# Optimization experiments

Measured on AMD Instinct MI355X. Metric: run time of the kernel, lower is better.

## Reference

```python
import jax, jax.numpy as jnp
import numpy as np

DIM = 1024
CTX_DIM = 1024
HEADS = 16
HEAD_DIM = DIM // HEADS


def setup_inputs() -> dict:
    key = jax.random.key(0)
    ks = jax.random.split(key, 6)
    B, N, M = 4, 2048, 2048
    s = 0.02
    return {
        "x": jax.random.normal(ks[0], (B, N, DIM), dtype=jnp.float32),
        "context": jax.random.normal(ks[1], (B, M, CTX_DIM), dtype=jnp.float32),
        "Wq": jax.random.normal(ks[2], (DIM, DIM), dtype=jnp.float32) * s,
        "Wk": jax.random.normal(ks[3], (CTX_DIM, DIM), dtype=jnp.float32) * s,
        "Wv": jax.random.normal(ks[4], (CTX_DIM, DIM), dtype=jnp.float32) * s,
        "Wo": jax.random.normal(ks[5], (DIM, DIM), dtype=jnp.float32) * s,
        "bo": jnp.zeros((DIM,), dtype=jnp.float32),
    }


def reference(x, context, Wq, Wk, Wv, Wo, bo):
    B, N, C = x.shape
    scale = HEAD_DIM ** -0.5
    # projections then split heads: (B, H, N, Dh)
    q = (x @ Wq.T).reshape(B, N, HEADS, HEAD_DIM).transpose(0, 2, 1, 3)
    k = (context @ Wk.T).reshape(B, -1, HEADS, HEAD_DIM).transpose(0, 2, 1, 3)
    v = (context @ Wv.T).reshape(B, -1, HEADS, HEAD_DIM).transpose(0, 2, 1, 3)
    attn = jnp.einsum('bhnd,bhmd->bhnm', q, k) * scale
    attn = jax.nn.softmax(attn, axis=-1)
    out = jnp.einsum('bhnm,bhmd->bhnd', attn, v)
    out = out.transpose(0, 2, 1, 3).reshape(B, N, C)
    return out @ Wo.T + bo
```

## Files before the change

### kernel.cpp

```cpp
#include <hip/hip_runtime.h>
#include <hip/hip_bf16.h>
#include <stdint.h>

typedef __bf16 bf16x8 __attribute__((ext_vector_type(8)));
typedef float  f32x4  __attribute__((ext_vector_type(4)));

#define SEQ   2048
#define DIMV  1024
#define HEADS 16
#define HDIM  64
#define KD    1024

#define SCL 0.1803368801111204f
#define THRRAW 44.36f

static __device__ __forceinline__ unsigned short f2bf(float f) {
  union { float f; unsigned u; } v; v.f = f;
  unsigned r = (v.u + 0x7fffu + ((v.u >> 16) & 1u)) >> 16;
  return (unsigned short)r;
}

__global__ void cvt_kernel(const float* __restrict__ src,
                           ushort4* __restrict__ dst, int n4) {
  int i = blockIdx.x * 256 + threadIdx.x;
  if (i >= n4) return;
  float4 v = reinterpret_cast<const float4*>(src)[i];
  ushort4 o;
  o.x = f2bf(v.x); o.y = f2bf(v.y); o.z = f2bf(v.z); o.w = f2bf(v.w);
  dst[i] = o;
}

static __device__ __forceinline__ void gload_lds16(const unsigned short* g,
                                                   unsigned short* l) {
  __builtin_amdgcn_global_load_lds(
      (const __attribute__((address_space(1))) unsigned int*)g,
      (__attribute__((address_space(3))) unsigned int*)l, 16, 0, 0);
}

template <int MODE>
__global__ __launch_bounds__(256) void gemm_bt(
    const unsigned short* __restrict__ A,
    const unsigned short* __restrict__ B,
    void* __restrict__ Cv,
    const float* __restrict__ bias) {
  __shared__ unsigned short As[128 * 32];
  __shared__ unsigned short Bs[128 * 32];
  const int t = threadIdx.x;
  const int lane = t & 63, wave = t >> 6;
  const int fr = lane & 15, fq = lane >> 4;
  const int m0 = blockIdx.x * 128, n0 = blockIdx.y * 128;
  const int wm0 = (wave >> 1) * 64, wn0 = (wave & 1) * 64;

  const int srow = wave * 16 + (lane >> 2);
  const int scol = (lane & 3) * 8;
  const unsigned short* gA = A + (size_t)(m0 + srow) * KD + scol;
  const unsigned short* gB = B + (size_t)(n0 + srow) * KD + scol;
  unsigned short* lA = &As[srow * 32 + scol];
  unsigned short* lB = &Bs[srow * 32 + scol];

  f32x4 acc[4][4];
#pragma unroll
  for (int i = 0; i < 4; ++i)
#pragma unroll
    for (int j = 0; j < 4; ++j) acc[i][j] = (f32x4){0.f, 0.f, 0.f, 0.f};

  for (int k0 = 0;;) {
    gload_lds16(gA + k0, lA);
    gload_lds16(gA + (size_t)64 * KD + k0, lA + 64 * 32);
    gload_lds16(gB + k0, lB);
    gload_lds16(gB + (size_t)64 * KD + k0, lB + 64 * 32);
    __syncthreads();

    bf16x8 af[4], bfv[4];
#pragma unroll
    for (int mi = 0; mi < 4; ++mi)
      af[mi] = *(const bf16x8*)&As[(wm0 + mi * 16 + fr) * 32 + fq * 8];
#pragma unroll
    for (int nj = 0; nj < 4; ++nj)
      bfv[nj] = *(const bf16x8*)&Bs[(wn0 + nj * 16 + fr) * 32 + fq * 8];
#pragma unroll
    for (int mi = 0; mi < 4; ++mi)
#pragma unroll
      for (int nj = 0; nj < 4; ++nj)
        acc[mi][nj] = __builtin_amdgcn_mfma_f32_16x16x32_bf16(
            af[mi], bfv[nj], acc[mi][nj], 0, 0, 0);

    k0 += 32;
    if (k0 >= KD) break;
    __syncthreads();
  }

#pragma unroll
  for (int mi = 0; mi < 4; ++mi)
#pragma unroll
    for (int nj = 0; nj < 4; ++nj)
#pragma unroll
      for (int r = 0; r < 4; ++r) {
        const int gr = m0 + wm0 + mi * 16 + fq * 4 + r;
        const int gc = n0 + wn0 + nj * 16 + fr;
        const float v = acc[mi][nj][r];
        if (MODE == 0) {
          size_t off = (((size_t)(gr >> 11) * HEADS + (gc >> 6)) * SEQ +
                        (gr & 2047)) * HDIM + (gc & 63);
          ((unsigned short*)Cv)[off] = f2bf(v);
        } else if (MODE == 1) {
          size_t off = (size_t)(gc >> 11) * (DIMV * SEQ) + (size_t)gr * SEQ +
                       (gc & 2047);
          ((unsigned short*)Cv)[off] = f2bf(v);
        } else {
          ((float*)Cv)[(size_t)gr * DIMV + gc] = v + bias[gc];
        }
      }
}

__global__ __launch_bounds__(256) void attn_kernel(
    const unsigned short* __restrict__ q, const unsigned short* __restrict__ k,
    const unsigned short* __restrict__ vt, unsigned short* __restrict__ ao) {
  __shared__ unsigned short Pl[4][32 * 64];
  const int t = threadIdx.x, lane = t & 63, wave = t >> 6;
  const int fr = lane & 15, fq = lane >> 4;
  const int wg = blockIdx.x;
  const int xcd = wg & 7, idx = wg >> 3;
  const int bh = (xcd << 3) | (idx >> 4);
  const int qt = idx & 15;
  const int b = bh >> 4, h = bh & 15;
  const int qrow0 = qt * 128 + wave * 32;

  const unsigned short* qp = q + ((size_t)bh * SEQ + qrow0) * HDIM;
  const unsigned short* kp = k + (size_t)bh * SEQ * HDIM;
  const unsigned short* vp = vt + (size_t)b * (DIMV * SEQ) + (size_t)(h * HDIM) * SEQ;
  char* plw = (char*)&Pl[wave][0];

  bf16x8 qf[2][2];
#pragma unroll
  for (int mi = 0; mi < 2; ++mi)
#pragma unroll
    for (int kc = 0; kc < 2; ++kc)
      qf[mi][kc] = *(const bf16x8*)(qp + (size_t)(mi * 16 + fr) * HDIM + kc * 32 + fq * 8);

  f32x4 oacc[2][4];
  float m_s[2], m_o[2][4], lrow[2];
#pragma unroll
  for (int mi = 0; mi < 2; ++mi) {
#pragma unroll
    for (int dj = 0; dj < 4; ++dj) oacc[mi][dj] = (f32x4){0.f, 0.f, 0.f, 0.f};
    m_s[mi] = -1e30f; lrow[mi] = 0.f;
#pragma unroll
    for (int r = 0; r < 4; ++r) m_o[mi][r] = -1e30f;
  }

  for (int kb = 0; kb < SEQ; kb += 64) {
    bf16x8 kf[4][2], vf[4][2];
#pragma unroll
    for (int nj = 0; nj < 4; ++nj)
#pragma unroll
      for (int kc = 0; kc < 2; ++kc)
        kf[nj][kc] = *(const bf16x8*)(kp + (size_t)(kb + nj * 16 + fr) * HDIM + kc * 32 + fq * 8);
#pragma unroll
    for (int dj = 0; dj < 4; ++dj)
#pragma unroll
      for (int kc = 0; kc < 2; ++kc)
        vf[dj][kc] = *(const bf16x8*)(vp + (size_t)(dj * 16 + fr) * SEQ + kb + kc * 32 + fq * 8);

    f32x4 sacc[2][4];
#pragma unroll
    for (int mi = 0; mi < 2; ++mi)
#pragma unroll
      for (int nj = 0; nj < 4; ++nj) sacc[mi][nj] = (f32x4){0.f, 0.f, 0.f, 0.f};
    __builtin_amdgcn_s_setprio(1);
#pragma unroll
    for (int mi = 0; mi < 2; ++mi)
#pragma unroll
      for (int nj = 0; nj < 4; ++nj)
#pragma unroll
        for (int kc = 0; kc < 2; ++kc)
          sacc[mi][nj] = __builtin_amdgcn_mfma_f32_16x16x32_bf16(
              kf[nj][kc], qf[mi][kc], sacc[mi][nj], 0, 0, 0);
    __builtin_amdgcn_s_setprio(0);

#pragma unroll
    for (int mi = 0; mi < 2; ++mi) {
      float tmax = -1e30f;
#pragma unroll
      for (int nj = 0; nj < 4; ++nj)
#pragma unroll
        for (int r = 0; r < 4; ++r) tmax = fmaxf(tmax, sacc[mi][nj][r]);
      tmax = fmaxf(tmax, __shfl_xor(tmax, 16));
      tmax = fmaxf(tmax, __shfl_xor(tmax, 32));

      if (__any(tmax > m_s[mi] + THRRAW)) {
        const float mnew = fmaxf(m_s[mi], tmax);
        lrow[mi] *= exp2f((m_s[mi] - mnew) * SCL);
        m_s[mi] = mnew;
#pragma unroll
        for (int r = 0; r < 4; ++r) {
          const float t_o = __shfl(tmax, ((lane >> 4) << 2) + r);
          const float mo_new = fmaxf(m_o[mi][r], t_o);
          const float fo = exp2f((m_o[mi][r] - mo_new) * SCL);
          m_o[mi][r] = mo_new;
#pragma unroll
          for (int dj = 0; dj < 4; ++dj) oacc[mi][dj][r] *= fo;
        }
      }

      const float nm = m_s[mi] * SCL;
      float ls = 0.f;
      const int row = mi * 16 + fr;
#pragma unroll
      for (int nj = 0; nj < 4; ++nj) {
        float p0 = exp2f(__builtin_fmaf(sacc[mi][nj][0], SCL, -nm));
        float p1 = exp2f(__builtin_fmaf(sacc[mi][nj][1], SCL, -nm));
        float p2 = exp2f(__builtin_fmaf(sacc[mi][nj][2], SCL, -nm));
        float p3 = exp2f(__builtin_fmaf(sacc[mi][nj][3], SCL, -nm));
        ls += (p0 + p1) + (p2 + p3);
        unsigned lo = (unsigned)f2bf(p0) | ((unsigned)f2bf(p1) << 16);
        unsigned hi = (unsigned)f2bf(p2) | ((unsigned)f2bf(p3) << 16);
        const int colb = (nj * 16 + fq * 4) * 2;
        *(uint2*)(plw + ((row * 128 + colb) ^ ((row & 7) << 4))) =
            make_uint2(lo, hi);
      }
      lrow[mi] += ls;
    }

    bf16x8 pf[2][2];
#pragma unroll
    for (int mi = 0; mi < 2; ++mi)
#pragma unroll
      for (int kc = 0; kc < 2; ++kc) {
        const int row = mi * 16 + fr, colb = (kc * 32 + fq * 8) * 2;
        pf[mi][kc] = *(const bf16x8*)(plw + ((row * 128 + colb) ^ ((row & 7) << 4)));
      }
    __builtin_amdgcn_s_setprio(1);
#pragma unroll
    for (int mi = 0; mi < 2; ++mi)
#pragma unroll
      for (int dj = 0; dj < 4; ++dj)
#pragma unroll
        for (int kc = 0; kc < 2; ++kc)
          oacc[mi][dj] = __builtin_amdgcn_mfma_f32_16x16x32_bf16(
              pf[mi][kc], vf[dj][kc], oacc[mi][dj], 0, 0, 0);
    __builtin_amdgcn_s_setprio(0);
  }

#pragma unroll
  for (int mi = 0; mi < 2; ++mi) {
    float lt = lrow[mi];
    lt += __shfl_xor(lt, 16);
    lt += __shfl_xor(lt, 32);
#pragma unroll
    for (int r = 0; r < 4; ++r) {
      const float l_o = __shfl(lt, ((lane >> 4) << 2) + r);
      const float inv = 1.f / l_o;
      const size_t grow = (size_t)b * SEQ + qt * 128 + wave * 32 +
                          mi * 16 + fq * 4 + r;
#pragma unroll
      for (int dj = 0; dj < 4; ++dj) {
        const int col = h * HDIM + dj * 16 + fr;
        ao[grow * DIMV + col] = f2bf(oacc[mi][dj][r] * inv);
      }
    }
  }
}

extern "C" void kernel_launch(void* const* d_in, const int* in_sizes, int n_in,
                              void* d_out, int out_size, void* d_ws, size_t ws_size,
                              hipStream_t stream) {
  const float* x   = (const float*)d_in[0];
  const float* ctx = (const float*)d_in[1];
  const float* Wq  = (const float*)d_in[2];
  const float* Wk  = (const float*)d_in[3];
  const float* Wv  = (const float*)d_in[4];
  const float* Wo  = (const float*)d_in[5];
  const float* bo  = (const float*)d_in[6];

  char* ws = (char*)d_ws;
  unsigned short* xb  = (unsigned short*)(ws);
  unsigned short* cb  = (unsigned short*)(ws + 16777216);
  unsigned short* wqb = (unsigned short*)(ws + 33554432);
  unsigned short* wkb = (unsigned short*)(ws + 35651584);
  unsigned short* wvb = (unsigned short*)(ws + 37748736);
  unsigned short* wob = (unsigned short*)(ws + 39845888);
  unsigned short* qb  = (unsigned short*)(ws + 41943040);
  unsigned short* kb  = (unsigned short*)(ws + 58720256);
  unsigned short* vtb = (unsigned short*)(ws + 75497472);

  auto cvt = [&](const float* s, unsigned short* d, int n) {
    int n4 = n >> 2;
    cvt_kernel<<<(n4 + 255) / 256, 256, 0, stream>>>(s, (ushort4*)d, n4);
  };
  const int NTOK = 4 * SEQ;
  cvt(x,   xb,  NTOK * DIMV);
  cvt(ctx, cb,  NTOK * DIMV);
  cvt(Wq,  wqb, DIMV * DIMV);
  cvt(Wk,  wkb, DIMV * DIMV);
  cvt(Wv,  wvb, DIMV * DIMV);
  cvt(Wo,  wob, DIMV * DIMV);

  gemm_bt<0><<<dim3(64, 8), 256, 0, stream>>>(xb, wqb, qb, nullptr);
  gemm_bt<0><<<dim3(64, 8), 256, 0, stream>>>(cb, wkb, kb, nullptr);
  gemm_bt<1><<<dim3(8, 64), 256, 0, stream>>>(wvb, cb, vtb, nullptr);

  unsigned short* aob = xb;
  attn_kernel<<<dim3(1024), 256, 0, stream>>>(qb, kb, vtb, aob);

  gemm_bt<2><<<dim3(64, 8), 256, 0, stream>>>(aob, wob, (float*)d_out, bo);
}
```

Baseline: 473.0 us.

## Stage K/V tiles in double-buffered LDS shared by 8-wave attention blocks

```diff
diff --git a/kernel.cpp b/kernel.cpp
--- a/kernel.cpp
+++ b/kernel.cpp
@@ -113,24 +113,29 @@
       }
 }
 
-__global__ __launch_bounds__(256) void attn_kernel(
+__global__ __launch_bounds__(512) void attn_kernel(
     const unsigned short* __restrict__ q, const unsigned short* __restrict__ k,
     const unsigned short* __restrict__ vt, unsigned short* __restrict__ ao) {
-  __shared__ unsigned short Pl[4][32 * 64];
+  __shared__ unsigned short Ks[2][64 * 64];
+  __shared__ unsigned short Vs[2][64 * 64];
+  __shared__ unsigned short Pl[8][32 * 64];
   const int t = threadIdx.x, lane = t & 63, wave = t >> 6;
   const int fr = lane & 15, fq = lane >> 4;
   const int wg = blockIdx.x;
   const int xcd = wg & 7, idx = wg >> 3;
-  const int bh = (xcd << 3) | (idx >> 4);
-  const int qt = idx & 15;
+  const int bh = (xcd << 3) | (idx >> 3);
+  const int qt = idx & 7;
   const int b = bh >> 4, h = bh & 15;
-  const int qrow0 = qt * 128 + wave * 32;
+  const int qrow0 = qt * 256 + wave * 32;
 
   const unsigned short* qp = q + ((size_t)bh * SEQ + qrow0) * HDIM;
   const unsigned short* kp = k + (size_t)bh * SEQ * HDIM;
   const unsigned short* vp = vt + (size_t)b * (DIMV * SEQ) + (size_t)(h * HDIM) * SEQ;
   char* plw = (char*)&Pl[wave][0];
 
+  const int srow = t >> 3;
+  const int scolb = ((t & 7) << 4) ^ ((srow & 7) << 4);
+
   bf16x8 qf[2][2];
 #pragma unroll
   for (int mi = 0; mi < 2; ++mi)
@@ -149,34 +154,43 @@
     for (int r = 0; r < 4; ++r) m_o[mi][r] = -1e30f;
   }
 
-  for (int kb = 0; kb < SEQ; kb += 64) {
-    bf16x8 kf[4][2], vf[4][2];
-#pragma unroll
-    for (int nj = 0; nj < 4; ++nj)
-#pragma unroll
-      for (int kc = 0; kc < 2; ++kc)
-        kf[nj][kc] = *(const bf16x8*)(kp + (size_t)(kb + nj * 16 + fr) * HDIM + kc * 32 + fq * 8);
-#pragma unroll
-    for (int dj = 0; dj < 4; ++dj)
-#pragma unroll
-      for (int kc = 0; kc < 2; ++kc)
-        vf[dj][kc] = *(const bf16x8*)(vp + (size_t)(dj * 16 + fr) * SEQ + kb + kc * 32 + fq * 8);
+  gload_lds16(kp + (size_t)srow * HDIM + (scolb >> 1), &Ks[0][t * 8]);
+  gload_lds16(vp + (size_t)srow * SEQ + (scolb >> 1), &Vs[0][t * 8]);
+  __syncthreads();
+
+  int cur = 0;
+  for (int kb = 0; kb < SEQ; kb += 64, cur ^= 1) {
+    if (kb + 64 < SEQ) {
+      gload_lds16(kp + (size_t)(kb + 64 + srow) * HDIM + (scolb >> 1),
+                  &Ks[cur ^ 1][t * 8]);
+      gload_lds16(vp + (size_t)srow * SEQ + (kb + 64) + (scolb >> 1),
+                  &Vs[cur ^ 1][t * 8]);
+    }
+
+    const char* kls = (const char*)&Ks[cur][0];
+    const char* vls = (const char*)&Vs[cur][0];
 
     f32x4 sacc[2][4];
 #pragma unroll
     for (int mi = 0; mi < 2; ++mi)
 #pragma unroll
       for (int nj = 0; nj < 4; ++nj) sacc[mi][nj] = (f32x4){0.f, 0.f, 0.f, 0.f};
-    __builtin_amdgcn_s_setprio(1);
-#pragma unroll
-    for (int mi = 0; mi < 2; ++mi)
+#pragma unroll
+    for (int kc = 0; kc < 2; ++kc) {
+      bf16x8 kf[4];
 #pragma unroll
       for (int nj = 0; nj < 4; ++nj)
-#pragma unroll
-        for (int kc = 0; kc < 2; ++kc)
+        kf[nj] = *(const bf16x8*)(kls + (nj * 16 + fr) * 128 +
+                                  ((kc * 64 + fq * 16) ^ ((fr & 7) << 4)));
+      __builtin_amdgcn_s_setprio(1);
+#pragma unroll
+      for (int mi = 0; mi < 2; ++mi)
+#pragma unroll
+        for (int nj = 0; nj < 4; ++nj)
           sacc[mi][nj] = __builtin_amdgcn_mfma_f32_16x16x32_bf16(
-              kf[nj][kc], qf[mi][kc], sacc[mi][nj], 0, 0, 0);
-    __builtin_amdgcn_s_setprio(0);
+              kf[nj], qf[mi][kc], sacc[mi][nj], 0, 0, 0);
+      __builtin_amdgcn_s_setprio(0);
+    }
 
 #pragma unroll
     for (int mi = 0; mi < 2; ++mi) {
@@ -230,16 +244,24 @@
         const int row = mi * 16 + fr, colb = (kc * 32 + fq * 8) * 2;
         pf[mi][kc] = *(const bf16x8*)(plw + ((row * 128 + colb) ^ ((row & 7) << 4)));
       }
-    __builtin_amdgcn_s_setprio(1);
-#pragma unroll
-    for (int mi = 0; mi < 2; ++mi)
+#pragma unroll
+    for (int kc = 0; kc < 2; ++kc) {
+      bf16x8 vf[4];
 #pragma unroll
       for (int dj = 0; dj < 4; ++dj)
-#pragma unroll
-        for (int kc = 0; kc < 2; ++kc)
+        vf[dj] = *(const bf16x8*)(vls + (dj * 16 + fr) * 128 +
+                                  ((kc * 64 + fq * 16) ^ ((fr & 7) << 4)));
+      __builtin_amdgcn_s_setprio(1);
+#pragma unroll
+      for (int mi = 0; mi < 2; ++mi)
+#pragma unroll
+        for (int dj = 0; dj < 4; ++dj)
           oacc[mi][dj] = __builtin_amdgcn_mfma_f32_16x16x32_bf16(
-              pf[mi][kc], vf[dj][kc], oacc[mi][dj], 0, 0, 0);
-    __builtin_amdgcn_s_setprio(0);
+              pf[mi][kc], vf[dj], oacc[mi][dj], 0, 0, 0);
+      __builtin_amdgcn_s_setprio(0);
+    }
+
+    __syncthreads();
   }
 
 #pragma unroll
@@ -251,7 +273,7 @@
     for (int r = 0; r < 4; ++r) {
       const float l_o = __shfl(lt, ((lane >> 4) << 2) + r);
       const float inv = 1.f / l_o;
-      const size_t grow = (size_t)b * SEQ + qt * 128 + wave * 32 +
+      const size_t grow = (size_t)b * SEQ + qt * 256 + wave * 32 +
                           mi * 16 + fq * 4 + r;
 #pragma unroll
       for (int dj = 0; dj < 4; ++dj) {
@@ -301,7 +323,7 @@
   gemm_bt<1><<<dim3(8, 64), 256, 0, stream>>>(wvb, cb, vtb, nullptr);
 
   unsigned short* aob = xb;
-  attn_kernel<<<dim3(1024), 256, 0, stream>>>(qb, kb, vtb, aob);
+  attn_kernel<<<dim3(512), 512, 0, stream>>>(qb, kb, vtb, aob);
 
   gemm_bt<2><<<dim3(64, 8), 256, 0, stream>>>(aob, wob, (float*)d_out, bo);
 }
```

Measured after the change: 406.5 us. 14.1% less time.
